# Performance work log

Hardware: AMD Instinct MI355X
Metric: run time of the kernel (lower is better)

## Reference

```python
import jax, jax.numpy as jnp
import numpy as np

N = 8192       # number of points
C = 16         # num_colors (size of color distribution)
DIM = 2        # spatial dim (GeometricLoss(dim=2))


def setup_inputs() -> dict:
    key = jax.random.key(0)
    k1, k2 = jax.random.split(key)
    outputs = jax.random.normal(k1, (N, C), dtype=jnp.float32)
    points = jax.random.normal(k2, (N, DIM), dtype=jnp.float32)
    return {"outputs": outputs, "points": points, "k": 5}


def reference(outputs, points, k):
    # cdist(points, points) via the squared-norm expansion (avoids [N,N,dim] tensor)
    sq = jnp.sum(points * points, axis=1)                      # [N]
    d2 = sq[:, None] + sq[None, :] - 2.0 * (points @ points.T)  # [N,N]
    dist = jnp.sqrt(jnp.maximum(d2, 0.0))
    # k+1 smallest distances per row; drop self (distance 0)
    _, idx = jax.lax.top_k(-dist, k + 1)                        # [N,k+1]
    idx = idx[:, 1:]                                            # [N,k]
    neighbor_outputs = outputs[idx]                             # [N,k,C] gather
    # ||out_i - out_j|| over color dim, mean over all (i, neighbor) pairs
    differences = jnp.linalg.norm(outputs[:, None, :] - neighbor_outputs, axis=2)
    return differences.mean()
```

## Files before the change

kernel.cpp:

```cpp
#include <hip/hip_runtime.h>


static constexpr int NPTS    = 8192;
static constexpr int KNN     = 5;
static constexpr int CH      = 16;
static constexpr int QPB     = 4;
static constexpr int THREADS = 256;
static constexpr int NBLK    = NPTS / QPB;
static constexpr int CAP     = 128;
static constexpr int NF4     = NPTS / 2;
static constexpr int ITERS   = NF4 / THREADS;

__device__ __forceinline__ unsigned long long shfl_xor_u64(unsigned long long v, int m) {
    unsigned int lo = (unsigned int)v;
    unsigned int hi = (unsigned int)(v >> 32);
    lo = __shfl_xor(lo, m, 64);
    hi = __shfl_xor(hi, m, 64);
    return ((unsigned long long)hi << 32) | lo;
}

__device__ __forceinline__ float rfl(float x) {
    return __uint_as_float(__builtin_amdgcn_readfirstlane(__float_as_uint(x)));
}

__global__ __launch_bounds__(256, 2) void knn_loss_kernel(
        const float* __restrict__ outputs,
        const float* __restrict__ points,
        float* __restrict__ partial) {
    const int tid   = threadIdx.x;
    const int wave  = tid >> 6;
    const int lane  = tid & 63;
    const int qbase = blockIdx.x * QPB;

    const float2* __restrict__ pts2 = (const float2*)points;
    const float4* __restrict__ pts4 = (const float4*)points;
    const float FINF = __int_as_float(0x7f800000);

    float pix[QPB], piy[QPB], sqi[QPB];
    #pragma unroll
    for (int q = 0; q < QPB; ++q) {
        const float2 pq = pts2[qbase + q];
        pix[q] = rfl(pq.x); piy[q] = rfl(pq.y);
        sqi[q] = rfl(fmaf(pix[q], pix[q], piy[q] * piy[q]));
    }

    float4 p[ITERS];
    #pragma unroll
    for (int u = 0; u < ITERS; ++u)
        p[u] = pts4[u * THREADS + tid];

    float acc[QPB];
    #pragma unroll
    for (int q = 0; q < QPB; ++q) acc[q] = FINF;
    #pragma unroll
    for (int u = 0; u < ITERS; ++u) {
        const float hA = 0.5f * fmaf(p[u].x, p[u].x, p[u].y * p[u].y);
        const float hB = 0.5f * fmaf(p[u].z, p[u].z, p[u].w * p[u].w);
        #pragma unroll
        for (int q = 0; q < QPB; ++q) {
            const float eA = fmaf(-pix[q], p[u].x, fmaf(-piy[q], p[u].y, hA));
            const float eB = fmaf(-pix[q], p[u].z, fmaf(-piy[q], p[u].w, hB));
            acc[q] = fminf(fminf(acc[q], eA), eB);
        }
    }

    __shared__ float thrmin[QPB][THREADS];
    __shared__ unsigned long long buf[QPB][CAP];
    __shared__ int cnt[QPB];
    __shared__ float Ts[QPB];
    __shared__ float red[QPB];

    #pragma unroll
    for (int q = 0; q < QPB; ++q)
        thrmin[q][tid] = acc[q];
    if (tid < QPB) cnt[tid] = 0;
    __syncthreads();

    {
        float v = thrmin[wave][lane];
        #pragma unroll
        for (int r = 1; r < THREADS / 64; ++r)
            v = fminf(v, thrmin[wave][lane + r * 64]);
        float T = 0.0f;
        #pragma unroll
        for (int t = 0; t < KNN + 1; ++t) {
            float m = v;
            #pragma unroll
            for (int d = 1; d < 64; d <<= 1) m = fminf(m, __shfl_xor(m, d, 64));
            if (v == m) v = FINF;
            T = m;
        }
        if (lane == 0) Ts[wave] = T;
    }
    __syncthreads();

    float Tq[QPB];
    #pragma unroll
    for (int q = 0; q < QPB; ++q) Tq[q] = rfl(Ts[q]);

    #pragma unroll
    for (int u = 0; u < ITERS; ++u) {
        const int jpair = u * THREADS + tid;
        const float hA = 0.5f * fmaf(p[u].x, p[u].x, p[u].y * p[u].y);
        const float hB = 0.5f * fmaf(p[u].z, p[u].z, p[u].w * p[u].w);
        #pragma unroll
        for (int q = 0; q < QPB; ++q) {
            const float eA = fmaf(-pix[q], p[u].x, fmaf(-piy[q], p[u].y, hA));
            const float eB = fmaf(-pix[q], p[u].z, fmaf(-piy[q], p[u].w, hB));
            if (fminf(eA, eB) <= Tq[q]) {
                if (eA <= Tq[q]) {
                    const float d2 = fmaxf(fmaf(2.0f, eA, sqi[q]), 0.0f);
                    const int pos = atomicAdd(&cnt[q], 1);
                    if (pos < CAP)
                        buf[q][pos] = ((unsigned long long)__float_as_uint(d2) << 32)
                                      | (unsigned int)(2 * jpair);
                }
                if (eB <= Tq[q]) {
                    const float d2 = fmaxf(fmaf(2.0f, eB, sqi[q]), 0.0f);
                    const int pos = atomicAdd(&cnt[q], 1);
                    if (pos < CAP)
                        buf[q][pos] = ((unsigned long long)__float_as_uint(d2) << 32)
                                      | (unsigned int)(2 * jpair + 1);
                }
            }
        }
    }
    __syncthreads();

    const unsigned long long INF64 = ~0ull;
    const int n = min(cnt[wave], CAP);
    unsigned long long a  = (lane      < n) ? buf[wave][lane]      : INF64;
    unsigned long long b2 = (lane + 64 < n) ? buf[wave][lane + 64] : INF64;
    if (b2 < a) { unsigned long long t = a; a = b2; b2 = t; }

    unsigned int myj = 0;
    int active = 0;
    #pragma unroll
    for (int t = 0; t < KNN + 1; ++t) {
        unsigned long long m = a;
        #pragma unroll
        for (int d = 1; d < 64; d <<= 1) {
            const unsigned long long x = shfl_xor_u64(m, d);
            if (x < m) m = x;
        }
        if (a == m) { a = b2; b2 = INF64; }
        if (t >= 1 && lane == t) { myj = (unsigned int)m; active = 1; }
    }

    float nrm = 0.0f;
    if (active) {
        const float4* oi = (const float4*)(outputs + (size_t)(qbase + wave) * CH);
        const float4* oj = (const float4*)(outputs + (size_t)myj * CH);
        float s = 0.0f;
        #pragma unroll
        for (int c = 0; c < 4; ++c) {
            const float4 x = oi[c], y = oj[c];
            const float dx = x.x - y.x, dy = x.y - y.y;
            const float dz = x.z - y.z, dw = x.w - y.w;
            s += dx * dx + dy * dy + dz * dz + dw * dw;
        }
        nrm = sqrtf(s);
    }
    #pragma unroll
    for (int d = 1; d < 64; d <<= 1) nrm += __shfl_xor(nrm, d, 64);

    if (lane == 0) red[wave] = nrm;
    __syncthreads();
    if (tid == 0) {
        float s = 0.0f;
        #pragma unroll
        for (int wv = 0; wv < QPB; ++wv) s += red[wv];
        partial[blockIdx.x] = s;
    }
}

__global__ __launch_bounds__(256) void finalize_kernel(
        const float* __restrict__ partial, float* __restrict__ out) {
    double s = 0.0;
    for (int idx = threadIdx.x; idx < NBLK; idx += 256) s += (double)partial[idx];
    #pragma unroll
    for (int d = 1; d < 64; d <<= 1) s += __shfl_xor(s, d, 64);
    __shared__ double lds[4];
    const int wave = threadIdx.x >> 6;
    const int lane = threadIdx.x & 63;
    if (lane == 0) lds[wave] = s;
    __syncthreads();
    if (threadIdx.x == 0)
        out[0] = (float)((lds[0] + lds[1] + lds[2] + lds[3]) /
                         (double)((long long)NPTS * KNN));
}

extern "C" void kernel_launch(void* const* d_in, const int* in_sizes, int n_in,
                              void* d_out, int out_size, void* d_ws, size_t ws_size,
                              hipStream_t stream) {
    const float* outputs = (const float*)d_in[0];
    const float* points  = (const float*)d_in[1];
    float* partial = (float*)d_ws;
    float* out = (float*)d_out;

    knn_loss_kernel<<<NBLK, THREADS, 0, stream>>>(outputs, points, partial);
    finalize_kernel<<<1, 256, 0, stream>>>(partial, out);
}
```

Baseline: 90.04 us.

## Stream point batches instead of caching all in registers; fuse final reduction via atomics

Rather than holding all 16 float4 point pairs per thread in registers for both passes, each pass now reloads points in batches of four, which cuts register pressure and may raise occupancy at the cost of reading the points array twice (it is L2-resident). The separate finalize kernel is removed. Each block instead atomically adds its scaled partial sum into the output, which is zeroed with a memset first. This saves one kernel launch but makes the float summation order nondeterministic and drops the double-precision accumulation.

```diff
diff --git a/kernel.cpp b/kernel.cpp
--- a/kernel.cpp
+++ b/kernel.cpp
@@ -10,6 +10,8 @@
 static constexpr int CAP     = 128;
 static constexpr int NF4     = NPTS / 2;
 static constexpr int ITERS   = NF4 / THREADS;
+static constexpr int BAT     = 4;
+static constexpr int NB      = ITERS / BAT;
 
 __device__ __forceinline__ unsigned long long shfl_xor_u64(unsigned long long v, int m) {
     unsigned int lo = (unsigned int)v;
@@ -26,7 +28,7 @@
 __global__ __launch_bounds__(256, 2) void knn_loss_kernel(
         const float* __restrict__ outputs,
         const float* __restrict__ points,
-        float* __restrict__ partial) {
+        float* __restrict__ out) {
     const int tid   = threadIdx.x;
     const int wave  = tid >> 6;
     const int lane  = tid & 63;
@@ -44,23 +46,25 @@
         sqi[q] = rfl(fmaf(pix[q], pix[q], piy[q] * piy[q]));
     }
 
-    float4 p[ITERS];
-    #pragma unroll
-    for (int u = 0; u < ITERS; ++u)
-        p[u] = pts4[u * THREADS + tid];
-
     float acc[QPB];
     #pragma unroll
     for (int q = 0; q < QPB; ++q) acc[q] = FINF;
-    #pragma unroll
-    for (int u = 0; u < ITERS; ++u) {
-        const float hA = 0.5f * fmaf(p[u].x, p[u].x, p[u].y * p[u].y);
-        const float hB = 0.5f * fmaf(p[u].z, p[u].z, p[u].w * p[u].w);
+
+    for (int b = 0; b < NB; ++b) {
+        float4 p[BAT];
         #pragma unroll
-        for (int q = 0; q < QPB; ++q) {
-            const float eA = fmaf(-pix[q], p[u].x, fmaf(-piy[q], p[u].y, hA));
-            const float eB = fmaf(-pix[q], p[u].z, fmaf(-piy[q], p[u].w, hB));
-            acc[q] = fminf(fminf(acc[q], eA), eB);
+        for (int u = 0; u < BAT; ++u)
+            p[u] = pts4[(b * BAT + u) * THREADS + tid];
+        #pragma unroll
+        for (int u = 0; u < BAT; ++u) {
+            const float hA = 0.5f * fmaf(p[u].x, p[u].x, p[u].y * p[u].y);
+            const float hB = 0.5f * fmaf(p[u].z, p[u].z, p[u].w * p[u].w);
+            #pragma unroll
+            for (int q = 0; q < QPB; ++q) {
+                const float eA = fmaf(-pix[q], p[u].x, fmaf(-piy[q], p[u].y, hA));
+                const float eB = fmaf(-pix[q], p[u].z, fmaf(-piy[q], p[u].w, hB));
+                acc[q] = fminf(fminf(acc[q], eA), eB);
+            }
         }
     }
 
@@ -98,29 +102,35 @@
     #pragma unroll
     for (int q = 0; q < QPB; ++q) Tq[q] = rfl(Ts[q]);
 
-    #pragma unroll
-    for (int u = 0; u < ITERS; ++u) {
-        const int jpair = u * THREADS + tid;
-        const float hA = 0.5f * fmaf(p[u].x, p[u].x, p[u].y * p[u].y);
-        const float hB = 0.5f * fmaf(p[u].z, p[u].z, p[u].w * p[u].w);
+    for (int b = 0; b < NB; ++b) {
+        float4 p[BAT];
         #pragma unroll
-        for (int q = 0; q < QPB; ++q) {
-            const float eA = fmaf(-pix[q], p[u].x, fmaf(-piy[q], p[u].y, hA));
-            const float eB = fmaf(-pix[q], p[u].z, fmaf(-piy[q], p[u].w, hB));
-            if (fminf(eA, eB) <= Tq[q]) {
-                if (eA <= Tq[q]) {
-                    const float d2 = fmaxf(fmaf(2.0f, eA, sqi[q]), 0.0f);
-                    const int pos = atomicAdd(&cnt[q], 1);
-                    if (pos < CAP)
-                        buf[q][pos] = ((unsigned long long)__float_as_uint(d2) << 32)
-                                      | (unsigned int)(2 * jpair);
-                }
-                if (eB <= Tq[q]) {
-                    const float d2 = fmaxf(fmaf(2.0f, eB, sqi[q]), 0.0f);
-                    const int pos = atomicAdd(&cnt[q], 1);
-                    if (pos < CAP)
-                        buf[q][pos] = ((unsigned long long)__float_as_uint(d2) << 32)
-                                      | (unsigned int)(2 * jpair + 1);
+        for (int u = 0; u < BAT; ++u)
+            p[u] = pts4[(b * BAT + u) * THREADS + tid];
+        #pragma unroll
+        for (int u = 0; u < BAT; ++u) {
+            const int jpair = (b * BAT + u) * THREADS + tid;
+            const float hA = 0.5f * fmaf(p[u].x, p[u].x, p[u].y * p[u].y);
+            const float hB = 0.5f * fmaf(p[u].z, p[u].z, p[u].w * p[u].w);
+            #pragma unroll
+            for (int q = 0; q < QPB; ++q) {
+                const float eA = fmaf(-pix[q], p[u].x, fmaf(-piy[q], p[u].y, hA));
+                const float eB = fmaf(-pix[q], p[u].z, fmaf(-piy[q], p[u].w, hB));
+                if (fminf(eA, eB) <= Tq[q]) {
+                    if (eA <= Tq[q]) {
+                        const float d2 = fmaxf(fmaf(2.0f, eA, sqi[q]), 0.0f);
+                        const int pos = atomicAdd(&cnt[q], 1);
+                        if (pos < CAP)
+                            buf[q][pos] = ((unsigned long long)__float_as_uint(d2) << 32)
+                                          | (unsigned int)(2 * jpair);
+                    }
+                    if (eB <= Tq[q]) {
+                        const float d2 = fmaxf(fmaf(2.0f, eB, sqi[q]), 0.0f);
+                        const int pos = atomicAdd(&cnt[q], 1);
+                        if (pos < CAP)
+                            buf[q][pos] = ((unsigned long long)__float_as_uint(d2) << 32)
+                                          | (unsigned int)(2 * jpair + 1);
+                    }
                 }
             }
         }
@@ -170,24 +180,8 @@
         float s = 0.0f;
         #pragma unroll
         for (int wv = 0; wv < QPB; ++wv) s += red[wv];
-        partial[blockIdx.x] = s;
+        atomicAdd(out, s * (1.0f / (float)(NPTS * KNN)));
     }
-}
-
-__global__ __launch_bounds__(256) void finalize_kernel(
-        const float* __restrict__ partial, float* __restrict__ out) {
-    double s = 0.0;
-    for (int idx = threadIdx.x; idx < NBLK; idx += 256) s += (double)partial[idx];
-    #pragma unroll
-    for (int d = 1; d < 64; d <<= 1) s += __shfl_xor(s, d, 64);
-    __shared__ double lds[4];
-    const int wave = threadIdx.x >> 6;
-    const int lane = threadIdx.x & 63;
-    if (lane == 0) lds[wave] = s;
-    __syncthreads();
-    if (threadIdx.x == 0)
-        out[0] = (float)((lds[0] + lds[1] + lds[2] + lds[3]) /
-                         (double)((long long)NPTS * KNN));
 }
 
 extern "C" void kernel_launch(void* const* d_in, const int* in_sizes, int n_in,
@@ -195,9 +189,8 @@
                               hipStream_t stream) {
     const float* outputs = (const float*)d_in[0];
     const float* points  = (const float*)d_in[1];
-    float* partial = (float*)d_ws;
     float* out = (float*)d_out;
 
-    knn_loss_kernel<<<NBLK, THREADS, 0, stream>>>(outputs, points, partial);
-    finalize_kernel<<<1, 256, 0, stream>>>(partial, out);
+    hipMemsetAsync(out, 0, sizeof(float), stream);
+    knn_loss_kernel<<<NBLK, THREADS, 0, stream>>>(outputs, points, out);
 }
```

Result: slower. 96.82 us (+7.5%).
